# Kernel tuning notes

Hardware: AMD Instinct MI355X
Metric: run time of the kernel (lower is better)

Reference implementation:

```python
import jax, jax.numpy as jnp
import numpy as np

GH, GW = 8, 8  # hypernetwork patch grid
EPS = 1e-5


def image_coords(b, h, w, dtype):
    # matches get_image_coordinates: channel0 = x (varies along W), channel1 = y (varies along H)
    xs = jnp.linspace(-1.0, 1.0, w, dtype=dtype)
    ys = jnp.linspace(-1.0, 1.0, h, dtype=dtype)
    X = jnp.broadcast_to(xs[None, :], (h, w))
    Y = jnp.broadcast_to(ys[:, None], (h, w))
    g = jnp.stack([X, Y], axis=0)  # [2,H,W]
    return jnp.broadcast_to(g[None], (b, 2, h, w))


def im2col3(x):
    # reflect-pad 3x3 im2col -> [B,C,9,H,W]
    H, W = x.shape[2], x.shape[3]
    xp = jnp.pad(x, ((0, 0), (0, 0), (1, 1), (1, 1)), mode='reflect')
    cols = [xp[:, :, i:i + H, j:j + W] for i in range(3) for j in range(3)]
    return jnp.stack(cols, axis=2)


def meta_dw3(x, wsig):
    # depthwise 3x3 conv with per-patch weights. wsig: [B, C*9, GH, GW]
    B, C, H, W = x.shape
    p, q = H // GH, W // GW
    cols = im2col3(x).reshape(B, C, 9, GH, p, GW, q)
    Wd = wsig.reshape(B, C, 9, GH, GW)
    out = jnp.einsum('bctuivj,bctuv->bcuivj', cols, Wd)
    return out.reshape(B, C, H, W)


def meta_pw(x, wsig, out_nc):
    # pointwise 1x1 conv with per-patch weights. wsig: [B, out_nc*C, GH, GW]
    B, C, H, W = x.shape
    p, q = H // GH, W // GW
    xr = x.reshape(B, C, GH, p, GW, q)
    Wp = wsig.reshape(B, out_nc, C, GH, GW)
    out = jnp.einsum('bcuivj,bocuv->bouivj', xr, Wp)
    return out.reshape(B, out_nc, H, W)


def batch_norm(x, g, b):
    m = jnp.mean(x, (0, 2, 3), keepdims=True)
    v = jnp.var(x, (0, 2, 3), keepdims=True)
    return (x - m) * jax.lax.rsqrt(v + EPS) * g[None, :, None, None] + b[None, :, None, None]


def relu6(x):
    return jnp.clip(x, 0.0, 6.0)


def hpir(x, wsig, out_nc, g_dw, b_dw, g_pw, b_pw):
    # HyperPatchInvertedResidual, expand_ratio=1, stride=1, in_nc != out_nc -> no residual
    C = x.shape[1]
    n_dw = C * 9
    h = relu6(batch_norm(meta_dw3(x, wsig[:, :n_dw]), g_dw, b_dw))
    h = batch_norm(meta_pw(h, wsig[:, n_dw:n_dw + out_nc * C], out_nc), g_pw, b_pw)
    return h


def resize_bilinear(p, hw):
    B, C = p.shape[0], p.shape[1]
    return jax.image.resize(p, (B, C, hw[0], hw[1]), method='bilinear')


def decoder_forward(x_img, f0, f1, w0, w1, w2,
                    g_dw0, b_dw0, g_pw0, b_pw0,
                    g_dw1, b_dw1, g_pw1, b_pw1,
                    g_dw2, b_dw2, g_pw2, b_pw2):
    feats = [x_img, f0, f1]  # [img] + features[:-1]
    level_w = [w0, w1, w2]
    level_out = [64, 32, 21]
    bn_p = [(g_dw0, b_dw0, g_pw0, b_pw0),
            (g_dw1, b_dw1, g_pw1, b_pw1),
            (g_dw2, b_dw2, g_pw2, b_pw2)]
    p = None
    for level in range(3):
        f = feats[-level - 1]
        if p is None:
            p = f
        else:
            if p.shape[2:] != f.shape[2:]:
                p = resize_bilinear(p, f.shape[2:])
            p = jnp.concatenate([f, p], axis=1)
        B, _, H, W = p.shape
        p = jnp.concatenate([image_coords(B, H, W, p.dtype), p], axis=1)
        g_dw, b_dw, g_pw, b_pw = bn_p[level]
        p = hpir(p, level_w[level], level_out[level], g_dw, b_dw, g_pw, b_pw)
    return p


def setup_inputs() -> dict:
    key = jax.random.key(0)
    ks = jax.random.split(key, 8)
    inp = {
        'x_img': jax.random.normal(ks[0], (4, 3, 256, 256), jnp.float32),
        'f0': jax.random.normal(ks[1], (4, 32, 64, 64), jnp.float32),
        'f1': jax.random.normal(ks[2], (4, 64, 32, 32), jnp.float32),
        'w0': jax.random.normal(ks[3], (4, 4818, 8, 8), jnp.float32) * 0.1,
        'w1': jax.random.normal(ks[4], (4, 4018, 8, 8), jnp.float32) * 0.1,
        'w2': jax.random.normal(ks[5], (4, 1110, 8, 8), jnp.float32) * 0.1,
    }
    for name, c in [('dw0', 66), ('pw0', 64), ('dw1', 98), ('pw1', 32), ('dw2', 37), ('pw2', 21)]:
        inp['g_' + name] = jnp.ones((c,), jnp.float32)
        inp['b_' + name] = jnp.zeros((c,), jnp.float32)
    return inp


def reference(x_img, f0, f1, w0, w1, w2,
              g_dw0, b_dw0, g_pw0, b_pw0,
              g_dw1, b_dw1, g_pw1, b_pw1,
              g_dw2, b_dw2, g_pw2, b_pw2):
    return decoder_forward(x_img, f0, f1, w0, w1, w2,
                           g_dw0, b_dw0, g_pw0, b_pw0,
                           g_dw1, b_dw1, g_pw1, b_pw1,
                           g_dw2, b_dw2, g_pw2, b_pw2)
```

## Files before the change

### kernel.cpp

```cpp
#include <hip/hip_runtime.h>

#define EPS 1e-5f

__device__ __forceinline__ int reflect_idx(int i, int n) {
    if (i < 0) return -i;
    if (i >= n) return 2 * n - 2 - i;
    return i;
}

__device__ __forceinline__ float bilin(const float* __restrict__ pb, int Hp, float sy, float sx) {
    int y0 = (int)floorf(sy), x0 = (int)floorf(sx);
    float fy = sy - y0, fx = sx - x0;
    int y0c = min(max(y0, 0), Hp - 1), y1c = min(max(y0 + 1, 0), Hp - 1);
    int x0c = min(max(x0, 0), Hp - 1), x1c = min(max(x0 + 1, 0), Hp - 1);
    float v00 = pb[y0c * Hp + x0c], v01 = pb[y0c * Hp + x1c];
    float v10 = pb[y1c * Hp + x0c], v11 = pb[y1c * Hp + x1c];
    return v00 * (1 - fy) * (1 - fx) + v01 * (1 - fy) * fx
         + v10 * fy * (1 - fx) + v11 * fy * fx;
}

template <int C>
__device__ __forceinline__ void reduce_ss_wide(const float* __restrict__ part,
                                               const float* __restrict__ g,
                                               const float* __restrict__ bb,
                                               float* ss, float* scratch,
                                               float invN, int tid) {
    constexpr int G = 256 / C;
    int grp = tid / C;
    int c = tid - grp * C;
    if (grp < G) {
        float s1 = 0.f, s2 = 0.f;
        for (int s = grp; s < 64; s += G) {
            s1 += part[s * 2 * C + 2 * c];
            s2 += part[s * 2 * C + 2 * c + 1];
        }
        scratch[grp * 2 * C + 2 * c] = s1;
        scratch[grp * 2 * C + 2 * c + 1] = s2;
    }
    __syncthreads();
    if (tid < C) {
        float s1 = 0.f, s2 = 0.f;
#pragma unroll
        for (int gg = 0; gg < G; ++gg) {
            s1 += scratch[gg * 2 * C + 2 * tid];
            s2 += scratch[gg * 2 * C + 2 * tid + 1];
        }
        float m = s1 * invN;
        float var = s2 * invN - m * m;
        float sc = g[tid] * rsqrtf(var + EPS);
        ss[2 * tid] = sc;
        ss[2 * tid + 1] = bb[tid] - m * sc;
    }
    __syncthreads();
}

__global__ __launch_bounds__(256)
void wtrans_kernel(const float* __restrict__ w2, float* __restrict__ wT) {
    int uv = blockIdx.x & 63, b = blockIdx.x >> 6;
    const float* src = w2 + (size_t)b * 1110 * 64 + uv;
    float* dst = wT + ((size_t)(b * 64 + uv)) * 1110;
    for (int i = threadIdx.x; i < 1110; i += 256) dst[i] = src[(size_t)i * 64];
}

template <int LEVEL, bool WRITE>
__global__ __launch_bounds__(256)
void fused_dw_kernel(const float* __restrict__ feat, const float* __restrict__ prev,
                     const float* __restrict__ part_prev, const float* __restrict__ g_prev,
                     const float* __restrict__ b_prev, float invN_prev,
                     const float* __restrict__ wsig,
                     float* __restrict__ out, float* __restrict__ part) {
    constexpr int C    = LEVEL == 0 ? 66 : 98;
    constexpr int H    = LEVEL == 0 ? 32 : 64;
    constexpr int TILE = 16;
    constexpr int NT   = H / TILE;
    constexpr int PXPT = (TILE * TILE) / 256;
    constexpr int WC   = LEVEL == 0 ? 4818 : 4018;
    constexpr int NF   = LEVEL == 0 ? 64 : 32;
    constexpr int Hp   = LEVEL == 1 ? 32 : 64;
    constexpr int Cp   = LEVEL == 1 ? 64 : 32;
    constexpr int P    = H / 8;
    constexpr float SC = 0.5f;
    constexpr int HS   = TILE + 2;
    constexpr int PSS  = (LEVEL == 0) ? 2 : 2 * Cp;

    __shared__ float sh[HS * HS];
    __shared__ float pssl[PSS];
    __shared__ float scratch[512];
    int tid = threadIdx.x, bid = blockIdx.x;
    int tile = bid % (NT * NT);
    int c = (bid / (NT * NT)) % C;
    int b = bid / (NT * NT * C);
    int ty0 = (tile / NT) * TILE, tx0 = (tile % NT) * TILE;

    if constexpr (LEVEL != 0) {
        reduce_ss_wide<Cp>(part_prev, g_prev, b_prev, pssl, scratch, invN_prev, tid);
    }

    for (int i = tid; i < HS * HS; i += 256) {
        int h = reflect_idx(ty0 - 1 + i / HS, H);
        int w = reflect_idx(tx0 - 1 + i % HS, H);
        float val;
        if (c == 0)      val = -1.f + 2.f * w / (H - 1);
        else if (c == 1) val = -1.f + 2.f * h / (H - 1);
        else if (c < 2 + NF) val = feat[((size_t)(b * NF + c - 2) * H + h) * H + w];
        else {
            int o = c - 2 - NF;
            const float* pb = prev + (size_t)(b * Cp + o) * Hp * Hp;
            float raw = bilin(pb, Hp, (h + 0.5f) * SC - 0.5f, (w + 0.5f) * SC - 0.5f);
            val = raw * pssl[2 * o] + pssl[2 * o + 1];
        }
        sh[i] = val;
    }
    __syncthreads();

    float s1 = 0.f, s2 = 0.f;
    float* ob = out + (((size_t)(b * C + c)) * H + ty0) * H + tx0;
    float wreg[9];
    if constexpr (TILE == P) {
        const float* wb = wsig + ((size_t)(b * WC + c * 9)) * 64 + (ty0 / P) * 8 + (tx0 / P);
#pragma unroll
        for (int t = 0; t < 9; ++t) wreg[t] = wb[(size_t)t * 64];
    }
#pragma unroll
    for (int k = 0; k < PXPT; ++k) {
        int px = tid + k * 256;
        int tyy = px / TILE, txx = px % TILE;
        if constexpr (TILE != P) {
            int u = (ty0 + tyy) / P, vv = (tx0 + txx) / P;
            const float* wb = wsig + ((size_t)(b * WC + c * 9)) * 64 + u * 8 + vv;
#pragma unroll
            for (int t = 0; t < 9; ++t) wreg[t] = wb[(size_t)t * 64];
        }
        float acc = 0.f;
#pragma unroll
        for (int t = 0; t < 9; ++t)
            acc += wreg[t] * sh[(tyy + t / 3) * HS + txx + t % 3];
        if constexpr (WRITE) ob[tyy * H + txx] = acc;
        s1 += acc; s2 += acc * acc;
    }
#pragma unroll
    for (int off = 32; off; off >>= 1) {
        s1 += __shfl_xor(s1, off);
        s2 += __shfl_xor(s2, off);
    }
    __shared__ float r1[4], r2[4];
    int wave = tid >> 6;
    if ((tid & 63) == 0) { r1[wave] = s1; r2[wave] = s2; }
    __syncthreads();
    if (tid == 0) {
        int slot = bid & 63;
        atomicAdd(&part[slot * 2 * C + 2 * c],     r1[0] + r1[1] + r1[2] + r1[3]);
        atomicAdd(&part[slot * 2 * C + 2 * c + 1], r2[0] + r2[1] + r2[2] + r2[3]);
    }
}

__global__ __launch_bounds__(256)
void dw2_col_kernel(const float* __restrict__ ximg, const float* __restrict__ prev,
                    const float* __restrict__ part_prev, const float* __restrict__ g_prev,
                    const float* __restrict__ b_prev,
                    const float* __restrict__ wT,
                    float* __restrict__ out, float* __restrict__ part) {
    const int C = 37, H = 256, W = 256, Hp = 64, Cp = 32;
    const int S = 260;
    __shared__ float sh[10 * S];
    __shared__ float pssl[64];
    __shared__ float lwv[72];
    __shared__ float scratch[512];
    __shared__ float r1[4], r2[4];

    int tid = threadIdx.x, bid = blockIdx.x;
    int rb = bid & 31;
    int c  = (bid >> 5) % C;
    int b  = bid / (32 * C);
    int ty0 = rb * 8;
    int u = rb >> 2;

    if (tid < 72) {
        int v = tid / 9, t = tid - v * 9;
        lwv[tid] = wT[((size_t)(b * 64 + u * 8 + v)) * 1110 + c * 9 + t];
    }
    reduce_ss_wide<32>(part_prev, g_prev, b_prev, pssl, scratch, 1.f / 16384.f, tid);

    const float* pb = (c >= 5) ? prev + (size_t)(b * Cp + (c - 5)) * Hp * Hp : nullptr;
    const float* xrow = (c >= 2 && c < 5) ? ximg + (size_t)(b * 3 + c - 2) * H * W : nullptr;
    float cx = -1.f + tid * (2.f / 255.f);
    float sxm = (tid + 0.5f) * 0.25f - 0.5f;
    int x0m = (int)floorf(sxm);
    float fxm = sxm - x0m;
    int x0cm = min(max(x0m, 0), Hp - 1), x1cm = min(max(x0m + 1, 0), Hp - 1);

#pragma unroll
    for (int r = 0; r < 10; ++r) {
        int h = reflect_idx(ty0 - 1 + r, H);
        float val;
        if (c == 0)      val = cx;
        else if (c == 1) val = -1.f + h * (2.f / 255.f);
        else if (c < 5)  val = xrow[h * W + tid];
        else {
            float sy = (h + 0.5f) * 0.25f - 0.5f;
            int y0 = (int)floorf(sy);
            float fy = sy - y0;
            int y0c = min(max(y0, 0), Hp - 1), y1c = min(max(y0 + 1, 0), Hp - 1);
            const float* q0 = pb + y0c * Hp;
            const float* q1 = pb + y1c * Hp;
            float a0 = q0[x0cm] + (q0[x1cm] - q0[x0cm]) * fxm;
            float a1 = q1[x0cm] + (q1[x1cm] - q1[x0cm]) * fxm;
            float raw = a0 + (a1 - a0) * fy;
            val = raw * pssl[2 * (c - 5)] + pssl[2 * (c - 5) + 1];
        }
        sh[r * S + tid + 1] = val;
    }
    if (tid < 20) {
        int r = tid >> 1, side = tid & 1;
        int wimg = side ? 254 : 1;
        int h = reflect_idx(ty0 - 1 + r, H);
        float val;
        if (c == 0)      val = -1.f + wimg * (2.f / 255.f);
        else if (c == 1) val = -1.f + h * (2.f / 255.f);
        else if (c < 5)  val = xrow[h * W + wimg];
        else {
            float sx = (wimg + 0.5f) * 0.25f - 0.5f;
            int x0 = (int)floorf(sx); float fx = sx - x0;
            int x0c = min(max(x0, 0), Hp - 1), x1c = min(max(x0 + 1, 0), Hp - 1);
            float sy = (h + 0.5f) * 0.25f - 0.5f;
            int y0 = (int)floorf(sy); float fy = sy - y0;
            int y0c = min(max(y0, 0), Hp - 1), y1c = min(max(y0 + 1, 0), Hp - 1);
            const float* q0 = pb + y0c * Hp;
            const float* q1 = pb + y1c * Hp;
            float a0 = q0[x0c] + (q0[x1c] - q0[x0c]) * fx;
            float a1 = q1[x0c] + (q1[x1c] - q1[x0c]) * fx;
            float raw = a0 + (a1 - a0) * fy;
            val = raw * pssl[2 * (c - 5)] + pssl[2 * (c - 5) + 1];
        }
        sh[r * S + (side ? 257 : 0)] = val;
    }
    __syncthreads();

    int t = tid;
    int v = t >> 5;
    float wr[9];
#pragma unroll
    for (int tap = 0; tap < 9; ++tap) wr[tap] = lwv[v * 9 + tap];

    float px[8];
#pragma unroll
    for (int k = 0; k < 8; ++k) px[k] = 0.f;

#pragma unroll
    for (int r = 0; r < 10; ++r) {
        float L = sh[r * S + t];
        float M = sh[r * S + t + 1];
        float R = sh[r * S + t + 2];
#pragma unroll
        for (int dr = 0; dr < 3; ++dr) {
            int k = r - dr;
            if (k >= 0 && k < 8)
                px[k] += wr[dr * 3] * L + wr[dr * 3 + 1] * M + wr[dr * 3 + 2] * R;
        }
    }

    float* ob = out + (((size_t)(b * C + c)) * H + ty0) * W + t;
    float s1 = 0.f, s2 = 0.f;
#pragma unroll
    for (int k = 0; k < 8; ++k) {
        ob[k * W] = px[k];
        s1 += px[k]; s2 += px[k] * px[k];
    }
#pragma unroll
    for (int off = 32; off; off >>= 1) {
        s1 += __shfl_xor(s1, off);
        s2 += __shfl_xor(s2, off);
    }
    int wave = tid >> 6;
    if ((tid & 63) == 0) { r1[wave] = s1; r2[wave] = s2; }
    __syncthreads();
    if (tid == 0) {
        int slot = bid & 63;
        atomicAdd(&part[slot * 2 * C + 2 * c],     r1[0] + r1[1] + r1[2] + r1[3]);
        atomicAdd(&part[slot * 2 * C + 2 * c + 1], r2[0] + r2[1] + r2[2] + r2[3]);
    }
}

template <int C, int ONC, int H, int PX_T, int OC_T>
__global__ __launch_bounds__(256)
void pw_small_kernel(const float* __restrict__ x, const float* __restrict__ wsig,
                     const float* __restrict__ part_in, const float* __restrict__ g,
                     const float* __restrict__ bb, float invN,
                     float* __restrict__ out, float* __restrict__ part, int WC, int ndw) {
    constexpr int P = H / 8;
    constexpr int OC_I = ONC / OC_T;
    __shared__ float lw[ONC * C];
    __shared__ float lx[C * PX_T];
    __shared__ float ssl[2 * C];
    __shared__ float scratch[512];
    int tid = threadIdx.x, bid = blockIdx.x;
    int uv = bid & 63, b = bid >> 6;
    int u = uv >> 3, v = uv & 7;

    const size_t wbase = ((size_t)b * WC + ndw) * 64 + uv;
    for (int i = tid; i < ONC * C; i += 256) lw[i] = wsig[wbase + (size_t)i * 64];
    reduce_ss_wide<C>(part_in, g, bb, ssl, scratch, invN, tid);

    for (int i = tid; i < C * PX_T; i += 256) {
        int c = i / PX_T, pxl = i % PX_T;
        int h = u * P + pxl / P, w = v * P + pxl % P;
        float xv = x[(((size_t)b * C + c) * H + h) * H + w];
        lx[i] = fminf(fmaxf(xv * ssl[2 * c] + ssl[2 * c + 1], 0.f), 6.f);
    }
    __syncthreads();

    int px_id = tid % PX_T, oc_id = tid / PX_T;
    int h = u * P + px_id / P, w = v * P + px_id % P;
    float acc[OC_I];
#pragma unroll
    for (int oi = 0; oi < OC_I; ++oi) acc[oi] = 0.f;
    for (int c = 0; c < C; ++c) {
        float xv = lx[c * PX_T + px_id];
#pragma unroll
        for (int oi = 0; oi < OC_I; ++oi)
            acc[oi] += lw[(oc_id * OC_I + oi) * C + c] * xv;
    }
    float* ob = out + (((size_t)b * ONC) * H + h) * H + w;
#pragma unroll
    for (int oi = 0; oi < OC_I; ++oi)
        ob[(size_t)(oc_id * OC_I + oi) * H * H] = acc[oi];

    constexpr int GROUP = (PX_T < 64) ? PX_T : 64;
    int lane = tid & 63;
    int slot = bid & 63;
#pragma unroll
    for (int oi = 0; oi < OC_I; ++oi) {
        float s1 = acc[oi], s2 = acc[oi] * acc[oi];
#pragma unroll
        for (int off = GROUP / 2; off; off >>= 1) {
            s1 += __shfl_xor(s1, off);
            s2 += __shfl_xor(s2, off);
        }
        if ((lane & (GROUP - 1)) == 0) {
            int o = oc_id * OC_I + oi;
            atomicAdd(&part[slot * 2 * ONC + 2 * o], s1);
            atomicAdd(&part[slot * 2 * ONC + 2 * o + 1], s2);
        }
    }
}

__global__ __launch_bounds__(256)
void pw2_kernel(const float* __restrict__ x, const float* __restrict__ wT,
                const float* __restrict__ part_in, const float* __restrict__ g,
                const float* __restrict__ bb,
                float* __restrict__ out, float* __restrict__ part) {
    const int C = 37, ONC = 21, H = 256;
    __shared__ float lw[777];
    __shared__ float ssl[74];
    __shared__ float scratch[512];
    __shared__ float r1[4][ONC], r2[4][ONC];
    int tid = threadIdx.x, bid = blockIdx.x;
    int chunk = bid & 3;
    int uv = (bid >> 2) & 63;
    int b = bid >> 8;
    int y0 = (uv >> 3) * 32 + chunk * 8, x0 = (uv & 7) * 32;

    const float* wt = wT + ((size_t)(b * 64 + uv)) * 1110 + 333;
    for (int i = tid; i < 777; i += 256) lw[i] = wt[i];
    reduce_ss_wide<37>(part_in, g, bb, ssl, scratch, 1.f / 262144.f, tid);

    int row = tid >> 5, col = tid & 31;
    const float* xb = x + (((size_t)(b * C)) * H + y0 + row) * H + x0 + col;
    float acc[ONC];
#pragma unroll
    for (int o = 0; o < ONC; ++o) acc[o] = 0.f;

    for (int c = 0; c < C; ++c) {
        float xv = xb[(size_t)c * H * H];
        xv = fminf(fmaxf(xv * ssl[2 * c] + ssl[2 * c + 1], 0.f), 6.f);
#pragma unroll
        for (int o = 0; o < ONC; ++o)
            acc[o] += lw[o * C + c] * xv;
    }
    float* ob = out + (((size_t)(b * ONC)) * H + y0 + row) * H + x0 + col;
#pragma unroll
    for (int o = 0; o < ONC; ++o) ob[(size_t)o * H * H] = acc[o];

    int wave = tid >> 6, lane = tid & 63;
#pragma unroll
    for (int o = 0; o < ONC; ++o) {
        float s1 = acc[o], s2 = acc[o] * acc[o];
#pragma unroll
        for (int off = 32; off; off >>= 1) {
            s1 += __shfl_xor(s1, off);
            s2 += __shfl_xor(s2, off);
        }
        if (lane == 0) { r1[wave][o] = s1; r2[wave][o] = s2; }
    }
    __syncthreads();
    int slot = bid & 63;
    for (int o = tid; o < ONC; o += 256) {
        atomicAdd(&part[slot * 42 + 2 * o],     r1[0][o] + r1[1][o] + r1[2][o] + r1[3][o]);
        atomicAdd(&part[slot * 42 + 2 * o + 1], r2[0][o] + r2[1][o] + r2[2][o] + r2[3][o]);
    }
}

__global__ __launch_bounds__(256)
void finalbn_kernel(float* __restrict__ out, const float* __restrict__ part_in,
                    const float* __restrict__ g, const float* __restrict__ bb) {
    __shared__ float ssl[42];
    __shared__ float scratch[512];
    reduce_ss_wide<21>(part_in, g, bb, ssl, scratch, 1.f / 262144.f, threadIdx.x);
    const int total4 = 4 * 21 * 256 * 256 / 4;
    for (int idx = blockIdx.x * 256 + threadIdx.x; idx < total4; idx += gridDim.x * 256) {
        int c = (idx / (256 * 256 / 4)) % 21;
        float4 v = ((float4*)out)[idx];
        float sc = ssl[2 * c], sb = ssl[2 * c + 1];
        v.x = v.x * sc + sb; v.y = v.y * sc + sb; v.z = v.z * sc + sb; v.w = v.w * sc + sb;
        ((float4*)out)[idx] = v;
    }
}

extern "C" void kernel_launch(void* const* d_in, const int* in_sizes, int n_in,
                              void* d_out, int out_size, void* d_ws, size_t ws_size,
                              hipStream_t stream) {
    const float* x_img = (const float*)d_in[0];
    const float* f0    = (const float*)d_in[1];
    const float* f1    = (const float*)d_in[2];
    const float* w0    = (const float*)d_in[3];
    const float* w1    = (const float*)d_in[4];
    const float* w2    = (const float*)d_in[5];
    const float* g_dw0 = (const float*)d_in[6],  *b_dw0 = (const float*)d_in[7];
    const float* g_pw0 = (const float*)d_in[8],  *b_pw0 = (const float*)d_in[9];
    const float* g_dw1 = (const float*)d_in[10], *b_dw1 = (const float*)d_in[11];
    const float* g_pw1 = (const float*)d_in[12], *b_pw1 = (const float*)d_in[13];
    const float* g_dw2 = (const float*)d_in[14], *b_dw2 = (const float*)d_in[15];
    const float* g_pw2 = (const float*)d_in[16], *b_pw2 = (const float*)d_in[17];
    float* out = (float*)d_out;
    float* ws = (float*)d_ws;

    float* part_dw0 = ws;
    float* part_pw0 = ws + 8448;
    float* part_dw1 = ws + 16640;
    float* part_pw1 = ws + 29184;
    float* part_dw2 = ws + 33280;
    float* part_pw2 = ws + 38016;
    float* wT     = ws + 40704;
    float* pw0raw = ws + 324864;
    float* pw1raw = pw0raw + 262144;
    float* bigA   = pw1raw + 524288;

    hipMemsetAsync(ws, 0, 40704 * sizeof(float), stream);
    wtrans_kernel<<<256, 256, 0, stream>>>(w2, wT);

    fused_dw_kernel<0, true><<<4 * 66 * 4, 256, 0, stream>>>(
        f1, nullptr, nullptr, nullptr, nullptr, 0.f, w0, bigA, part_dw0);
    pw_small_kernel<66, 64, 32, 16, 16><<<256, 256, 0, stream>>>(
        bigA, w0, part_dw0, g_dw0, b_dw0, 1.f / 4096.f, pw0raw, part_pw0, 4818, 594);
    fused_dw_kernel<1, true><<<4 * 98 * 16, 256, 0, stream>>>(
        f0, pw0raw, part_pw0, g_pw0, b_pw0, 1.f / 4096.f, w1, bigA, part_dw1);
    pw_small_kernel<98, 32, 64, 64, 4><<<256, 256, 0, stream>>>(
        bigA, w1, part_dw1, g_dw1, b_dw1, 1.f / 16384.f, pw1raw, part_pw1, 4018, 882);
    dw2_col_kernel<<<4 * 37 * 32, 256, 0, stream>>>(
        x_img, pw1raw, part_pw1, g_pw1, b_pw1, wT, bigA, part_dw2);
    pw2_kernel<<<1024, 256, 0, stream>>>(bigA, wT, part_dw2, g_dw2, b_dw2, out, part_pw2);
    finalbn_kernel<<<1024, 256, 0, stream>>>(out, part_pw2, g_pw2, b_pw2);
}
```

Measured before the change: 157.8 us.

## Hoist BN stat reductions into tiny kernels and drop weight transpose

Each consumer kernel used to reduce the 64-slot partial BN sums for every block itself. That reduction now runs once per stage in a separate single-block red_kernel, and consumers read the precomputed scale/shift arrays. The wtrans_kernel is removed, so dw2 and pw2 read w2 directly with stride-64 gathers. finalbn becomes a one-element-per-thread grid. This removes redundant per-block reductions and an extra launch, but adds six tiny serial kernel launches and uncoalesced weight reads.

```diff
diff --git a/kernel.cpp b/kernel.cpp
--- a/kernel.cpp
+++ b/kernel.cpp
@@ -19,55 +19,10 @@
          + v10 * fy * (1 - fx) + v11 * fy * fx;
 }
 
-template <int C>
-__device__ __forceinline__ void reduce_ss_wide(const float* __restrict__ part,
-                                               const float* __restrict__ g,
-                                               const float* __restrict__ bb,
-                                               float* ss, float* scratch,
-                                               float invN, int tid) {
-    constexpr int G = 256 / C;
-    int grp = tid / C;
-    int c = tid - grp * C;
-    if (grp < G) {
-        float s1 = 0.f, s2 = 0.f;
-        for (int s = grp; s < 64; s += G) {
-            s1 += part[s * 2 * C + 2 * c];
-            s2 += part[s * 2 * C + 2 * c + 1];
-        }
-        scratch[grp * 2 * C + 2 * c] = s1;
-        scratch[grp * 2 * C + 2 * c + 1] = s2;
-    }
-    __syncthreads();
-    if (tid < C) {
-        float s1 = 0.f, s2 = 0.f;
-#pragma unroll
-        for (int gg = 0; gg < G; ++gg) {
-            s1 += scratch[gg * 2 * C + 2 * tid];
-            s2 += scratch[gg * 2 * C + 2 * tid + 1];
-        }
-        float m = s1 * invN;
-        float var = s2 * invN - m * m;
-        float sc = g[tid] * rsqrtf(var + EPS);
-        ss[2 * tid] = sc;
-        ss[2 * tid + 1] = bb[tid] - m * sc;
-    }
-    __syncthreads();
-}
-
-__global__ __launch_bounds__(256)
-void wtrans_kernel(const float* __restrict__ w2, float* __restrict__ wT) {
-    int uv = blockIdx.x & 63, b = blockIdx.x >> 6;
-    const float* src = w2 + (size_t)b * 1110 * 64 + uv;
-    float* dst = wT + ((size_t)(b * 64 + uv)) * 1110;
-    for (int i = threadIdx.x; i < 1110; i += 256) dst[i] = src[(size_t)i * 64];
-}
-
 template <int LEVEL, bool WRITE>
 __global__ __launch_bounds__(256)
 void fused_dw_kernel(const float* __restrict__ feat, const float* __restrict__ prev,
-                     const float* __restrict__ part_prev, const float* __restrict__ g_prev,
-                     const float* __restrict__ b_prev, float invN_prev,
-                     const float* __restrict__ wsig,
+                     const float* __restrict__ pss, const float* __restrict__ wsig,
                      float* __restrict__ out, float* __restrict__ part) {
     constexpr int C    = LEVEL == 0 ? 66 : 98;
     constexpr int H    = LEVEL == 0 ? 32 : 64;
@@ -76,25 +31,18 @@
     constexpr int PXPT = (TILE * TILE) / 256;
     constexpr int WC   = LEVEL == 0 ? 4818 : 4018;
     constexpr int NF   = LEVEL == 0 ? 64 : 32;
-    constexpr int Hp   = LEVEL == 1 ? 32 : 64;
-    constexpr int Cp   = LEVEL == 1 ? 64 : 32;
+    constexpr int Hp   = 32;
+    constexpr int Cp   = 64;
     constexpr int P    = H / 8;
     constexpr float SC = 0.5f;
     constexpr int HS   = TILE + 2;
-    constexpr int PSS  = (LEVEL == 0) ? 2 : 2 * Cp;
 
     __shared__ float sh[HS * HS];
-    __shared__ float pssl[PSS];
-    __shared__ float scratch[512];
     int tid = threadIdx.x, bid = blockIdx.x;
     int tile = bid % (NT * NT);
     int c = (bid / (NT * NT)) % C;
     int b = bid / (NT * NT * C);
     int ty0 = (tile / NT) * TILE, tx0 = (tile % NT) * TILE;
-
-    if constexpr (LEVEL != 0) {
-        reduce_ss_wide<Cp>(part_prev, g_prev, b_prev, pssl, scratch, invN_prev, tid);
-    }
 
     for (int i = tid; i < HS * HS; i += 256) {
         int h = reflect_idx(ty0 - 1 + i / HS, H);
@@ -107,7 +55,7 @@
             int o = c - 2 - NF;
             const float* pb = prev + (size_t)(b * Cp + o) * Hp * Hp;
             float raw = bilin(pb, Hp, (h + 0.5f) * SC - 0.5f, (w + 0.5f) * SC - 0.5f);
-            val = raw * pssl[2 * o] + pssl[2 * o + 1];
+            val = raw * pss[2 * o] + pss[2 * o + 1];
         }
         sh[i] = val;
     }
@@ -154,18 +102,33 @@
     }
 }
 
+__global__ void red_kernel(const float* __restrict__ part, const float* __restrict__ g,
+                           const float* __restrict__ bb, float* __restrict__ ss,
+                           int C, float invN) {
+    int c = threadIdx.x;
+    if (c >= C) return;
+    float s1 = 0.f, s2 = 0.f;
+#pragma unroll 8
+    for (int s = 0; s < 64; ++s) {
+        s1 += part[s * 2 * C + 2 * c];
+        s2 += part[s * 2 * C + 2 * c + 1];
+    }
+    float m = s1 * invN;
+    float var = s2 * invN - m * m;
+    float sc = g[c] * rsqrtf(var + EPS);
+    ss[2 * c] = sc;
+    ss[2 * c + 1] = bb[c] - m * sc;
+}
+
 __global__ __launch_bounds__(256)
 void dw2_col_kernel(const float* __restrict__ ximg, const float* __restrict__ prev,
-                    const float* __restrict__ part_prev, const float* __restrict__ g_prev,
-                    const float* __restrict__ b_prev,
-                    const float* __restrict__ wT,
+                    const float* __restrict__ pw1ss, const float* __restrict__ wsig,
                     float* __restrict__ out, float* __restrict__ part) {
-    const int C = 37, H = 256, W = 256, Hp = 64, Cp = 32;
+    const int C = 37, H = 256, W = 256, WC = 1110, Hp = 64, Cp = 32;
     const int S = 260;
     __shared__ float sh[10 * S];
     __shared__ float pssl[64];
     __shared__ float lwv[72];
-    __shared__ float scratch[512];
     __shared__ float r1[4], r2[4];
 
     int tid = threadIdx.x, bid = blockIdx.x;
@@ -175,19 +138,22 @@
     int ty0 = rb * 8;
     int u = rb >> 2;
 
+    if (tid < 64) pssl[tid] = pw1ss[tid];
     if (tid < 72) {
         int v = tid / 9, t = tid - v * 9;
-        lwv[tid] = wT[((size_t)(b * 64 + u * 8 + v)) * 1110 + c * 9 + t];
-    }
-    reduce_ss_wide<32>(part_prev, g_prev, b_prev, pssl, scratch, 1.f / 16384.f, tid);
-
-    const float* pb = (c >= 5) ? prev + (size_t)(b * Cp + (c - 5)) * Hp * Hp : nullptr;
+        lwv[tid] = wsig[((size_t)(b * WC + c * 9 + t)) * 64 + u * 8 + v];
+    }
+    __syncthreads();
+
+    const float* pb   = (c >= 5) ? prev + (size_t)(b * Cp + (c - 5)) * Hp * Hp : nullptr;
     const float* xrow = (c >= 2 && c < 5) ? ximg + (size_t)(b * 3 + c - 2) * H * W : nullptr;
     float cx = -1.f + tid * (2.f / 255.f);
     float sxm = (tid + 0.5f) * 0.25f - 0.5f;
     int x0m = (int)floorf(sxm);
     float fxm = sxm - x0m;
     int x0cm = min(max(x0m, 0), Hp - 1), x1cm = min(max(x0m + 1, 0), Hp - 1);
+    float psc = (c >= 5) ? pssl[2 * (c - 5)] : 0.f;
+    float psh = (c >= 5) ? pssl[2 * (c - 5) + 1] : 0.f;
 
 #pragma unroll
     for (int r = 0; r < 10; ++r) {
@@ -205,8 +171,7 @@
             const float* q1 = pb + y1c * Hp;
             float a0 = q0[x0cm] + (q0[x1cm] - q0[x0cm]) * fxm;
             float a1 = q1[x0cm] + (q1[x1cm] - q1[x0cm]) * fxm;
-            float raw = a0 + (a1 - a0) * fy;
-            val = raw * pssl[2 * (c - 5)] + pssl[2 * (c - 5) + 1];
+            val = (a0 + (a1 - a0) * fy) * psc + psh;
         }
         sh[r * S + tid + 1] = val;
     }
@@ -229,8 +194,7 @@
             const float* q1 = pb + y1c * Hp;
             float a0 = q0[x0c] + (q0[x1c] - q0[x0c]) * fx;
             float a1 = q1[x0c] + (q1[x1c] - q1[x0c]) * fx;
-            float raw = a0 + (a1 - a0) * fy;
-            val = raw * pssl[2 * (c - 5)] + pssl[2 * (c - 5) + 1];
+            val = (a0 + (a1 - a0) * fy) * psc + psh;
         }
         sh[r * S + (side ? 257 : 0)] = val;
     }
@@ -284,28 +248,23 @@
 template <int C, int ONC, int H, int PX_T, int OC_T>
 __global__ __launch_bounds__(256)
 void pw_small_kernel(const float* __restrict__ x, const float* __restrict__ wsig,
-                     const float* __restrict__ part_in, const float* __restrict__ g,
-                     const float* __restrict__ bb, float invN,
-                     float* __restrict__ out, float* __restrict__ part, int WC, int ndw) {
+                     const float* __restrict__ ss, float* __restrict__ out,
+                     float* __restrict__ part, int WC, int ndw) {
     constexpr int P = H / 8;
     constexpr int OC_I = ONC / OC_T;
     __shared__ float lw[ONC * C];
     __shared__ float lx[C * PX_T];
-    __shared__ float ssl[2 * C];
-    __shared__ float scratch[512];
     int tid = threadIdx.x, bid = blockIdx.x;
     int uv = bid & 63, b = bid >> 6;
     int u = uv >> 3, v = uv & 7;
 
     const size_t wbase = ((size_t)b * WC + ndw) * 64 + uv;
     for (int i = tid; i < ONC * C; i += 256) lw[i] = wsig[wbase + (size_t)i * 64];
-    reduce_ss_wide<C>(part_in, g, bb, ssl, scratch, invN, tid);
-
     for (int i = tid; i < C * PX_T; i += 256) {
         int c = i / PX_T, pxl = i % PX_T;
         int h = u * P + pxl / P, w = v * P + pxl % P;
         float xv = x[(((size_t)b * C + c) * H + h) * H + w];
-        lx[i] = fminf(fmaxf(xv * ssl[2 * c] + ssl[2 * c + 1], 0.f), 6.f);
+        lx[i] = fminf(fmaxf(xv * ss[2 * c] + ss[2 * c + 1], 0.f), 6.f);
     }
     __syncthreads();
 
@@ -345,14 +304,12 @@
 }
 
 __global__ __launch_bounds__(256)
-void pw2_kernel(const float* __restrict__ x, const float* __restrict__ wT,
-                const float* __restrict__ part_in, const float* __restrict__ g,
-                const float* __restrict__ bb,
+void pw2_kernel(const float* __restrict__ x, const float* __restrict__ wsig,
+                const float* __restrict__ dss,
                 float* __restrict__ out, float* __restrict__ part) {
-    const int C = 37, ONC = 21, H = 256;
+    const int C = 37, ONC = 21, H = 256, WC = 1110, NDW = 333;
     __shared__ float lw[777];
     __shared__ float ssl[74];
-    __shared__ float scratch[512];
     __shared__ float r1[4][ONC], r2[4][ONC];
     int tid = threadIdx.x, bid = blockIdx.x;
     int chunk = bid & 3;
@@ -360,9 +317,9 @@
     int b = bid >> 8;
     int y0 = (uv >> 3) * 32 + chunk * 8, x0 = (uv & 7) * 32;
 
-    const float* wt = wT + ((size_t)(b * 64 + uv)) * 1110 + 333;
-    for (int i = tid; i < 777; i += 256) lw[i] = wt[i];
-    reduce_ss_wide<37>(part_in, g, bb, ssl, scratch, 1.f / 262144.f, tid);
+    for (int i = tid; i < 777; i += 256) lw[i] = wsig[((size_t)(b * WC + NDW) + i) * 64 + uv];
+    if (tid < 74) ssl[tid] = dss[tid];
+    __syncthreads();
 
     int row = tid >> 5, col = tid & 31;
     const float* xb = x + (((size_t)(b * C)) * H + y0 + row) * H + x0 + col;
@@ -400,20 +357,15 @@
     }
 }
 
-__global__ __launch_bounds__(256)
-void finalbn_kernel(float* __restrict__ out, const float* __restrict__ part_in,
-                    const float* __restrict__ g, const float* __restrict__ bb) {
-    __shared__ float ssl[42];
-    __shared__ float scratch[512];
-    reduce_ss_wide<21>(part_in, g, bb, ssl, scratch, 1.f / 262144.f, threadIdx.x);
+__global__ void finalbn_kernel(float* __restrict__ out, const float* __restrict__ ss) {
+    int idx = blockIdx.x * 256 + threadIdx.x;
     const int total4 = 4 * 21 * 256 * 256 / 4;
-    for (int idx = blockIdx.x * 256 + threadIdx.x; idx < total4; idx += gridDim.x * 256) {
-        int c = (idx / (256 * 256 / 4)) % 21;
-        float4 v = ((float4*)out)[idx];
-        float sc = ssl[2 * c], sb = ssl[2 * c + 1];
-        v.x = v.x * sc + sb; v.y = v.y * sc + sb; v.z = v.z * sc + sb; v.w = v.w * sc + sb;
-        ((float4*)out)[idx] = v;
-    }
+    if (idx >= total4) return;
+    int c = (idx / (256 * 256 / 4)) % 21;
+    float4 v = ((float4*)out)[idx];
+    float sc = ss[2 * c], sb = ss[2 * c + 1];
+    v.x = v.x * sc + sb; v.y = v.y * sc + sb; v.z = v.z * sc + sb; v.w = v.w * sc + sb;
+    ((float4*)out)[idx] = v;
 }
 
 extern "C" void kernel_launch(void* const* d_in, const int* in_sizes, int n_in,
@@ -440,24 +392,34 @@
     float* part_pw1 = ws + 29184;
     float* part_dw2 = ws + 33280;
     float* part_pw2 = ws + 38016;
-    float* wT     = ws + 40704;
-    float* pw0raw = ws + 324864;
+    float* dw0ss = ws + 40704;
+    float* pw0ss = ws + 40836;
+    float* dw1ss = ws + 40964;
+    float* pw1ss = ws + 41160;
+    float* dw2ss = ws + 41224;
+    float* pw2ss = ws + 41298;
+    float* pw0raw = ws + 41344;
     float* pw1raw = pw0raw + 262144;
     float* bigA   = pw1raw + 524288;
 
     hipMemsetAsync(ws, 0, 40704 * sizeof(float), stream);
-    wtrans_kernel<<<256, 256, 0, stream>>>(w2, wT);
 
     fused_dw_kernel<0, true><<<4 * 66 * 4, 256, 0, stream>>>(
-        f1, nullptr, nullptr, nullptr, nullptr, 0.f, w0, bigA, part_dw0);
+        f1, nullptr, nullptr, w0, bigA, part_dw0);
+    red_kernel<<<1, 128, 0, stream>>>(part_dw0, g_dw0, b_dw0, dw0ss, 66, 1.f / 4096.f);
     pw_small_kernel<66, 64, 32, 16, 16><<<256, 256, 0, stream>>>(
-        bigA, w0, part_dw0, g_dw0, b_dw0, 1.f / 4096.f, pw0raw, part_pw0, 4818, 594);
+        bigA, w0, dw0ss, pw0raw, part_pw0, 4818, 594);
+    red_kernel<<<1, 128, 0, stream>>>(part_pw0, g_pw0, b_pw0, pw0ss, 64, 1.f / 4096.f);
     fused_dw_kernel<1, true><<<4 * 98 * 16, 256, 0, stream>>>(
-        f0, pw0raw, part_pw0, g_pw0, b_pw0, 1.f / 4096.f, w1, bigA, part_dw1);
+        f0, pw0raw, pw0ss, w1, bigA, part_dw1);
+    red_kernel<<<1, 128, 0, stream>>>(part_dw1, g_dw1, b_dw1, dw1ss, 98, 1.f / 16384.f);
     pw_small_kernel<98, 32, 64, 64, 4><<<256, 256, 0, stream>>>(
-        bigA, w1, part_dw1, g_dw1, b_dw1, 1.f / 16384.f, pw1raw, part_pw1, 4018, 882);
+        bigA, w1, dw1ss, pw1raw, part_pw1, 4018, 882);
+    red_kernel<<<1, 128, 0, stream>>>(part_pw1, g_pw1, b_pw1, pw1ss, 32, 1.f / 16384.f);
     dw2_col_kernel<<<4 * 37 * 32, 256, 0, stream>>>(
-        x_img, pw1raw, part_pw1, g_pw1, b_pw1, wT, bigA, part_dw2);
-    pw2_kernel<<<1024, 256, 0, stream>>>(bigA, wT, part_dw2, g_dw2, b_dw2, out, part_pw2);
-    finalbn_kernel<<<1024, 256, 0, stream>>>(out, part_pw2, g_pw2, b_pw2);
-}
+        x_img, pw1raw, pw1ss, w2, bigA, part_dw2);
+    red_kernel<<<1, 128, 0, stream>>>(part_dw2, g_dw2, b_dw2, dw2ss, 37, 1.f / 262144.f);
+    pw2_kernel<<<1024, 256, 0, stream>>>(bigA, w2, dw2ss, out, part_pw2);
+    red_kernel<<<1, 128, 0, stream>>>(part_pw2, g_pw2, b_pw2, pw2ss, 21, 1.f / 262144.f);
+    finalbn_kernel<<<5376, 256, 0, stream>>>(out, pw2ss);
+}
```

Result: faster. 145.6 us (-7.7%).
